# Optimization experiments

Hardware: AMD Instinct MI355X
Metric: run time of the kernel (lower is better)

The kernel has to match this reference:

```python
import jax, jax.numpy as jnp
import numpy as np

HIDDEN = 1024
EXPAND = 2
D_REC = HIDDEN * EXPAND
INTER = 4096
B, T = 4, 4096


def _rmsnorm(x, w, eps=1e-6):
    var = jnp.mean(x * x, axis=-1, keepdims=True)
    return x * jax.lax.rsqrt(var + eps) * w


def setup_inputs() -> dict:
    key = jax.random.key(0)
    ks = jax.random.split(key, 11)
    s = lambda fan: 1.0 / np.sqrt(fan)
    return {
        "x": jax.random.normal(ks[0], (B, T, HIDDEN), dtype=jnp.float32),
        "ln1_w": jnp.ones((HIDDEN,), dtype=jnp.float32),
        "ln2_w": jnp.ones((HIDDEN,), dtype=jnp.float32),
        "w_in": jax.random.normal(ks[1], (D_REC, HIDDEN), dtype=jnp.float32) * s(HIDDEN),
        "w_gate": jax.random.normal(ks[2], (D_REC, HIDDEN), dtype=jnp.float32) * s(HIDDEN),
        "a_param": jax.random.normal(ks[3], (D_REC,), dtype=jnp.float32) * 0.1,
        "w_a": jax.random.normal(ks[4], (D_REC, D_REC), dtype=jnp.float32) * s(D_REC),
        "w_out": jax.random.normal(ks[5], (HIDDEN, D_REC), dtype=jnp.float32) * s(D_REC),
        "w_mlp_gate": jax.random.normal(ks[6], (INTER, HIDDEN), dtype=jnp.float32) * s(HIDDEN),
        "w_mlp_up": jax.random.normal(ks[7], (INTER, HIDDEN), dtype=jnp.float32) * s(HIDDEN),
        "w_mlp_down": jax.random.normal(ks[8], (HIDDEN, INTER), dtype=jnp.float32) * s(INTER),
    }


def _hawk_scan(x_in, a):
    # x_in, a: [B, T, D_REC]; h_t = a_t*h_{t-1} + sqrt(1-a_t^2+eps)*x_t
    xs = jnp.moveaxis(x_in, 1, 0)  # [T, B, D]
    As = jnp.moveaxis(a, 1, 0)

    def step(state, inp):
        a_t, x_t = inp
        new = a_t * state + jnp.sqrt(1.0 - a_t * a_t + 1e-8) * x_t
        return new, new

    init = jnp.zeros(x_in.shape[::2], dtype=x_in.dtype)  # [B, D]
    _, ys = jax.lax.scan(step, init, (As, xs))
    return jnp.moveaxis(ys, 0, 1)  # [B, T, D]


def reference(x, ln1_w, ln2_w, w_in, w_gate, a_param, w_a, w_out,
              w_mlp_gate, w_mlp_up, w_mlp_down):
    h = _rmsnorm(x, ln1_w)
    x_in = h @ w_in.T                     # [B,T,D_REC]
    gate = jax.nn.sigmoid(h @ w_gate.T)
    a = jax.nn.sigmoid(a_param + x_in @ w_a.T)
    y = gate * _hawk_scan(x_in, a)
    x = x + y @ w_out.T
    h2 = _rmsnorm(x, ln2_w)
    mlp = (jax.nn.silu(h2 @ w_mlp_gate.T) * (h2 @ w_mlp_up.T)) @ w_mlp_down.T
    return x + mlp
```

## Files before the change

### kernel.cpp

```cpp
#include <hip/hip_runtime.h>
#include <cstdint>
#include <cmath>


typedef unsigned short u16;
typedef _Float16 f16;
typedef __bf16 bf16x8 __attribute__((ext_vector_type(8)));
typedef float  f32x4  __attribute__((ext_vector_type(4)));

#define HID   1024
#define DREC  2048
#define INTER 4096
#define BT    16384
#define TLEN  4096
#define NCHAN 8192
#define CHUNK 64
#define NCH   64
#define NPAIR 4096

__device__ __forceinline__ float b2f(u16 u) {
  union { unsigned int i; float f; } v; v.i = ((unsigned int)u) << 16; return v.f;
}
__device__ __forceinline__ u16 f2bf(float f) {
  unsigned int u = __builtin_bit_cast(unsigned int, f);
  u += 0x7FFFu + ((u >> 16) & 1u);
  return (u16)(u >> 16);
}
__device__ __forceinline__ float sigm(float x) { return 1.f / (1.f + expf(-x)); }

typedef __attribute__((address_space(1))) void as1_void;
typedef __attribute__((address_space(3))) void as3_void;
__device__ __forceinline__ void async16(const void* g, void* l) {
  __builtin_amdgcn_global_load_lds((as1_void*)g, (as3_void*)l, 16, 0, 0);
}

#define BARSYNC() do { __builtin_amdgcn_s_barrier(); __builtin_amdgcn_sched_barrier(0); } while (0)
#define LGKM0()   do { asm volatile("s_waitcnt lgkmcnt(0)" ::: "memory"); __builtin_amdgcn_sched_barrier(0); } while (0)
#define VMC(N)    do { asm volatile("s_waitcnt vmcnt(" #N ")" ::: "memory"); __builtin_amdgcn_sched_barrier(0); } while (0)
#define FENCE()   do { asm volatile("" ::: "memory"); __builtin_amdgcn_sched_barrier(0); } while (0)

__global__ void f2b_all(const float* s0, const float* s1, const float* s2,
                        const float* s3, const float* s4, const float* s5,
                        const float* s6,
                        u16* d0, u16* d1, u16* d2, u16* d3, u16* d4, u16* d5,
                        u16* d6) {
  int blk = blockIdx.x;
  const float* src; u16* dst; int rel;
  if      (blk < 2048)  { src = s0; dst = d0; rel = blk; }
  else if (blk < 4096)  { src = s1; dst = d1; rel = blk - 2048; }
  else if (blk < 8192)  { src = s2; dst = d2; rel = blk - 4096; }
  else if (blk < 10240) { src = s3; dst = d3; rel = blk - 8192; }
  else if (blk < 14336) { src = s4; dst = d4; rel = blk - 10240; }
  else if (blk < 18432) { src = s5; dst = d5; rel = blk - 14336; }
  else                  { src = s6; dst = d6; rel = blk - 18432; }
  int i = rel * 256 + threadIdx.x;
  float4 v = ((const float4*)src)[i];
  ushort4 o;
  o.x = f2bf(v.x); o.y = f2bf(v.y); o.z = f2bf(v.z); o.w = f2bf(v.w);
  ((ushort4*)dst)[i] = o;
}

__global__ void rmsnorm_kernel(const float* __restrict__ x, const float* __restrict__ w,
                               u16* __restrict__ out) {
  const int row = blockIdx.x;
  const int tid = threadIdx.x;
  float4 v = ((const float4*)(x + (size_t)row * HID))[tid];
  float ss = v.x * v.x + v.y * v.y + v.z * v.z + v.w * v.w;
#pragma unroll
  for (int o = 32; o > 0; o >>= 1) ss += __shfl_down(ss, o);
  __shared__ float red[4];
  const int lane = tid & 63, wv = tid >> 6;
  if (lane == 0) red[wv] = ss;
  __syncthreads();
  float tot = red[0] + red[1] + red[2] + red[3];
  float sc = rsqrtf(tot * (1.f / (float)HID) + 1e-6f);
  float4 wv4 = ((const float4*)w)[tid];
  ushort4 o;
  o.x = f2bf(v.x * sc * wv4.x); o.y = f2bf(v.y * sc * wv4.y);
  o.z = f2bf(v.z * sc * wv4.z); o.w = f2bf(v.w * sc * wv4.w);
  ((ushort4*)(out + (size_t)row * HID))[tid] = o;
}

__device__ __forceinline__ void stageG(const u16* __restrict__ g, int ldg,
                                       int rb, int k0, u16* lbase, int tid) {
#pragma unroll
  for (int i = 0; i < 2; ++i) {
    int p = i * 512 + tid;
    int r = p >> 3;
    int sg = (p & 7) ^ (r & 7);
    async16(g + (size_t)(rb + r) * ldg + (k0 + sg * 8), (char*)lbase + p * 16);
  }
}

__device__ __forceinline__ void readA4(bf16x8 (&af)[4][2], const u16* base,
                                       int rbase, int quad) {
#pragma unroll
  for (int i = 0; i < 4; ++i) {
    int r = rbase + i * 16;
#pragma unroll
    for (int ks = 0; ks < 2; ++ks)
      af[i][ks] = ((const bf16x8*)base)[r * 8 + ((ks * 4 + quad) ^ (r & 7))];
  }
}
__device__ __forceinline__ void readB2(bf16x8 (&bf)[2][2], const u16* base,
                                       int rbase, int quad) {
#pragma unroll
  for (int i = 0; i < 2; ++i) {
    int r = rbase + i * 16;
#pragma unroll
    for (int ks = 0; ks < 2; ++ks)
      bf[i][ks] = ((const bf16x8*)base)[r * 8 + ((ks * 4 + quad) ^ (r & 7))];
  }
}

template <int MI0, int NI0, int NA>
__device__ __forceinline__ void mfmaQ(f32x4 (&acc)[8][NA],
                                      const bf16x8 (&af)[4][2],
                                      const bf16x8 (&bf)[2][2]) {
  __builtin_amdgcn_s_setprio(1);
#pragma unroll
  for (int mi = 0; mi < 4; ++mi)
#pragma unroll
    for (int ni = 0; ni < 2; ++ni)
#pragma unroll
      for (int ks = 0; ks < 2; ++ks)
        acc[MI0 + mi][NI0 + ni] = __builtin_amdgcn_mfma_f32_16x16x32_bf16(
            af[mi][ks], bf[ni][ks], acc[MI0 + mi][NI0 + ni], 0, 0, 0);
  __builtin_amdgcn_s_setprio(0);
}

enum { EPI_LOGIT = 0, EPI_ADDF = 1 };

template <int EPI>
__global__ __launch_bounds__(512, 2)
void gemm256(const u16* __restrict__ A, const u16* __restrict__ W,
             int K, int N, int ldA, int ldW,
             float* outf, f16* outz, const float* auxf) {
  __shared__ u16 sA[2][16384];
  __shared__ u16 sB[2][16384];
  const int tid  = threadIdx.x;
  const int lane = tid & 63, wv = tid >> 6;
  const int wm   = wv >> 2, wn = wv & 3;
  const int lm   = lane & 15, quad = lane >> 4;
  const int row0 = blockIdx.x * 256, col0 = blockIdx.y * 256;
  const int NT   = K >> 6;

  f32x4 acc[8][4];
#pragma unroll
  for (int i = 0; i < 8; ++i)
#pragma unroll
    for (int j = 0; j < 4; ++j) acc[i][j] = (f32x4)0.f;

  stageG(W, ldW, col0,       0, sB[0],        tid);
  stageG(W, ldW, col0 + 128, 0, sB[0] + 8192, tid);
  stageG(A, ldA, row0,       0, sA[0],        tid);
  stageG(A, ldA, row0 + 128, 0, sA[0] + 8192, tid);
  FENCE();
  if (NT > 1) {
    stageG(W, ldW, col0,       64, sB[1],        tid);
    stageG(W, ldW, col0 + 128, 64, sB[1] + 8192, tid);
    stageG(A, ldA, row0,       64, sA[1],        tid);
    stageG(A, ldA, row0 + 128, 64, sA[1] + 8192, tid);
    VMC(8);
  } else {
    VMC(0);
  }
  BARSYNC();

  for (int t = 0; t < NT; ++t) {
    const int b = t & 1;
    const u16* Ab = sA[b];
    const u16* Bb = sB[b];
    bf16x8 af[4][2], bfL[2][2], bfH[2][2];
    const int kN = (t + 2) * 64;

    readA4(af, Ab, wm * 128 + lm, quad);
    readB2(bfL, Bb, wn * 64 + lm, quad);
    BARSYNC(); LGKM0();
    mfmaQ<0, 0>(acc, af, bfL);
    BARSYNC();

    readB2(bfH, Bb, wn * 64 + 32 + lm, quad);
    BARSYNC(); LGKM0();
    mfmaQ<0, 2>(acc, af, bfH);
    BARSYNC();

    readA4(af, Ab, wm * 128 + 64 + lm, quad);
    if (t + 2 < NT) {
      stageG(W, ldW, col0,       kN, (u16*)sB[b],        tid);
      stageG(W, ldW, col0 + 128, kN, (u16*)sB[b] + 8192, tid);
    }
    BARSYNC(); LGKM0();
    mfmaQ<4, 2>(acc, af, bfH);
    BARSYNC();

    if (t + 2 < NT) {
      stageG(A, ldA, row0,       kN, (u16*)sA[b],        tid);
      stageG(A, ldA, row0 + 128, kN, (u16*)sA[b] + 8192, tid);
    }
    mfmaQ<4, 0>(acc, af, bfL);
    if (t + 2 < NT) { VMC(8); } else { VMC(0); }
    BARSYNC();
  }

#pragma unroll
  for (int mi = 0; mi < 8; ++mi) {
    const int rb = row0 + wm * 128 + mi * 16 + quad * 4;
#pragma unroll
    for (int ni = 0; ni < 4; ++ni) {
      const int cg = col0 + wn * 64 + ni * 16 + lm;
      f32x4 v = acc[mi][ni];
#pragma unroll
      for (int rr = 0; rr < 4; ++rr) {
        size_t idx = (size_t)(rb + rr) * N + cg;
        if constexpr (EPI == EPI_LOGIT) {
          outz[idx] = (f16)(v[rr] + auxf[cg]);
        } else {
          outf[idx] = v[rr] + auxf[idx];
        }
      }
    }
  }
}

enum { EPI2_XG = 0, EPI2_SM = 1 };

template <int EPI>
__global__ __launch_bounds__(512, 2)
void gemm256d(const u16* __restrict__ A, const u16* __restrict__ W0,
              const u16* __restrict__ W1,
              int K, int N, int ldA, int ldW,
              u16* out0, u16* out1) {
  __shared__ u16 sA[2][16384];
  __shared__ u16 sB[2][16384];
  const int tid  = threadIdx.x;
  const int lane = tid & 63, wv = tid >> 6;
  const int wm   = wv >> 2, wn = wv & 3;
  const int lm   = lane & 15, quad = lane >> 4;
  const int row0 = blockIdx.x * 256, col0 = blockIdx.y * 128;
  const int NT   = K >> 6;

  f32x4 acc0[8][2], acc1[8][2];
#pragma unroll
  for (int i = 0; i < 8; ++i)
#pragma unroll
    for (int j = 0; j < 2; ++j) { acc0[i][j] = (f32x4)0.f; acc1[i][j] = (f32x4)0.f; }

  stageG(W0, ldW, col0,       0, sB[0],        tid);
  stageG(W1, ldW, col0,       0, sB[0] + 8192, tid);
  stageG(A,  ldA, row0,       0, sA[0],        tid);
  stageG(A,  ldA, row0 + 128, 0, sA[0] + 8192, tid);
  FENCE();
  if (NT > 1) {
    stageG(W0, ldW, col0,       64, sB[1],        tid);
    stageG(W1, ldW, col0,       64, sB[1] + 8192, tid);
    stageG(A,  ldA, row0,       64, sA[1],        tid);
    stageG(A,  ldA, row0 + 128, 64, sA[1] + 8192, tid);
    VMC(8);
  } else {
    VMC(0);
  }
  BARSYNC();

  for (int t = 0; t < NT; ++t) {
    const int b = t & 1;
    const u16* Ab = sA[b];
    const u16* Bb = sB[b];
    bf16x8 af[4][2], bf0[2][2], bf1[2][2];
    const int kN = (t + 2) * 64;

    readA4(af, Ab, wm * 128 + lm, quad);
    readB2(bf0, Bb, wn * 32 + lm, quad);
    BARSYNC(); LGKM0();
    mfmaQ<0, 0>(acc0, af, bf0);
    BARSYNC();

    readB2(bf1, Bb + 8192, wn * 32 + lm, quad);
    if (t + 2 < NT) stageG(W0, ldW, col0, kN, (u16*)sB[b], tid);
    BARSYNC(); LGKM0();
    mfmaQ<0, 0>(acc1, af, bf1);
    BARSYNC();

    readA4(af, Ab, wm * 128 + 64 + lm, quad);
    if (t + 2 < NT) stageG(W1, ldW, col0, kN, (u16*)sB[b] + 8192, tid);
    BARSYNC(); LGKM0();
    mfmaQ<4, 0>(acc1, af, bf1);
    BARSYNC();

    if (t + 2 < NT) {
      stageG(A, ldA, row0,       kN, (u16*)sA[b],        tid);
      stageG(A, ldA, row0 + 128, kN, (u16*)sA[b] + 8192, tid);
    }
    mfmaQ<4, 0>(acc0, af, bf0);
    if (t + 2 < NT) { VMC(8); } else { VMC(0); }
    BARSYNC();
  }

#pragma unroll
  for (int mi = 0; mi < 8; ++mi) {
    const int rb = row0 + wm * 128 + mi * 16 + quad * 4;
#pragma unroll
    for (int ni = 0; ni < 2; ++ni) {
      const int cg = col0 + wn * 32 + ni * 16 + lm;
#pragma unroll
      for (int rr = 0; rr < 4; ++rr) {
        size_t idx = (size_t)(rb + rr) * N + cg;
        float v0 = acc0[mi][ni][rr];
        float v1 = acc1[mi][ni][rr];
        if constexpr (EPI == EPI2_XG) {
          out0[idx] = f2bf(v0);
          out1[idx] = f2bf(sigm(v1));
        } else {
          out0[idx] = f2bf(v0 * sigm(v0) * v1);
        }
      }
    }
  }
}

__global__ void scan_phase1(const f16* __restrict__ z, const u16* __restrict__ xin,
                            float2* __restrict__ ch_h, float2* __restrict__ ch_p) {
  int gtid = blockIdx.x * 256 + threadIdx.x;
  int c = gtid >> 12;
  int pair = gtid & (NPAIR - 1);
  int b = pair >> 10;
  int d = (pair & 1023) * 2;
  size_t base = ((size_t)b * TLEN + (size_t)c * CHUNK) * DREC + d;
  float2 h = {0.f, 0.f}, P = {1.f, 1.f};
#pragma unroll 8
  for (int t = 0; t < CHUNK; ++t) {
    size_t i = base + (size_t)t * DREC;
    f16 z2[2]; *(uint32_t*)z2 = *(const uint32_t*)(z + i);
    u16 x2[2]; *(uint32_t*)x2 = *(const uint32_t*)(xin + i);
    float a0 = sigm((float)z2[0]), a1 = sigm((float)z2[1]);
    h.x = a0 * h.x + sqrtf(1.f - a0 * a0 + 1e-8f) * b2f(x2[0]);
    h.y = a1 * h.y + sqrtf(1.f - a1 * a1 + 1e-8f) * b2f(x2[1]);
    P.x *= a0; P.y *= a1;
  }
  ch_h[gtid] = h;
  ch_p[gtid] = P;
}

__global__ void scan_phase2(float2* __restrict__ ch_h, const float2* __restrict__ ch_p) {
  int pair = blockIdx.x * 256 + threadIdx.x;
  float2 H = {0.f, 0.f};
#pragma unroll
  for (int c = 0; c < NCH; ++c) {
    int i = c * NPAIR + pair;
    float2 he = ch_h[i];
    float2 P  = ch_p[i];
    ch_h[i] = H;
    H.x = he.x + P.x * H.x;
    H.y = he.y + P.y * H.y;
  }
}

__global__ void scan_phase3(const f16* __restrict__ z, const u16* __restrict__ xin,
                            u16* gate_y, const float2* __restrict__ ch_h) {
  int gtid = blockIdx.x * 256 + threadIdx.x;
  int c = gtid >> 12;
  int pair = gtid & (NPAIR - 1);
  int b = pair >> 10;
  int d = (pair & 1023) * 2;
  size_t base = ((size_t)b * TLEN + (size_t)c * CHUNK) * DREC + d;
  float2 h = ch_h[gtid];
#pragma unroll 8
  for (int t = 0; t < CHUNK; ++t) {
    size_t i = base + (size_t)t * DREC;
    f16 z2[2]; *(uint32_t*)z2 = *(const uint32_t*)(z + i);
    u16 x2[2]; *(uint32_t*)x2 = *(const uint32_t*)(xin + i);
    u16 g2[2]; *(uint32_t*)g2 = *(const uint32_t*)(gate_y + i);
    float a0 = sigm((float)z2[0]), a1 = sigm((float)z2[1]);
    h.x = a0 * h.x + sqrtf(1.f - a0 * a0 + 1e-8f) * b2f(x2[0]);
    h.y = a1 * h.y + sqrtf(1.f - a1 * a1 + 1e-8f) * b2f(x2[1]);
    u16 o2[2];
    o2[0] = f2bf(b2f(g2[0]) * h.x);
    o2[1] = f2bf(b2f(g2[1]) * h.y);
    *(uint32_t*)(gate_y + i) = *(uint32_t*)o2;
  }
}

extern "C" void kernel_launch(void* const* d_in, const int* in_sizes, int n_in,
                              void* d_out, int out_size, void* d_ws, size_t ws_size,
                              hipStream_t stream) {
  const float* x      = (const float*)d_in[0];
  const float* ln1    = (const float*)d_in[1];
  const float* ln2    = (const float*)d_in[2];
  const float* w_in   = (const float*)d_in[3];
  const float* w_gate = (const float*)d_in[4];
  const float* a_par  = (const float*)d_in[5];
  const float* w_a    = (const float*)d_in[6];
  const float* w_out  = (const float*)d_in[7];
  const float* w_mg   = (const float*)d_in[8];
  const float* w_mu   = (const float*)d_in[9];
  const float* w_md   = (const float*)d_in[10];
  float* out = (float*)d_out;
  char* ws = (char*)d_ws;

  const size_t MB = 1024ull * 1024ull;
  u16* wb_in  = (u16*)(ws + 0 * MB);
  u16* wb_gt  = (u16*)(ws + 4 * MB);
  u16* wb_a   = (u16*)(ws + 8 * MB);
  u16* wb_out = (u16*)(ws + 16 * MB);
  u16* wb_mg  = (u16*)(ws + 20 * MB);
  u16* wb_mu  = (u16*)(ws + 28 * MB);
  u16* wb_md  = (u16*)(ws + 36 * MB);
  u16* hbuf  = (u16*)(ws + 44 * MB);
  f16* zbuf  = (f16*)(ws + 44 * MB);
  u16* gateb = (u16*)(ws + 108 * MB);
  u16* mbuf  = (u16*)(ws + 108 * MB);
  float2* chh = (float2*)(ws + 0 * MB);
  float2* chp = (float2*)(ws + 2 * MB);
  u16* xinb = (u16*)d_out;

  f2b_all<<<22528, 256, 0, stream>>>(w_in, w_gate, w_a, w_out, w_mg, w_mu, w_md,
                                     wb_in, wb_gt, wb_a, wb_out, wb_mg, wb_mu, wb_md);

  rmsnorm_kernel<<<BT, 256, 0, stream>>>(x, ln1, hbuf);

  gemm256d<EPI2_XG><<<dim3(BT / 256, DREC / 128), 512, 0, stream>>>(
      hbuf, wb_in, wb_gt, HID, DREC, HID, HID, xinb, gateb);

  gemm256<EPI_LOGIT><<<dim3(BT / 256, DREC / 256), 512, 0, stream>>>(
      xinb, wb_a, DREC, DREC, DREC, DREC, nullptr, zbuf, a_par);

  scan_phase1<<<NCH * NPAIR / 256, 256, 0, stream>>>(zbuf, xinb, chh, chp);
  scan_phase2<<<NPAIR / 256, 256, 0, stream>>>(chh, chp);
  scan_phase3<<<NCH * NPAIR / 256, 256, 0, stream>>>(zbuf, xinb, gateb, chh);

  gemm256<EPI_ADDF><<<dim3(BT / 256, HID / 256), 512, 0, stream>>>(
      gateb, wb_out, DREC, HID, DREC, DREC, out, nullptr, x);

  rmsnorm_kernel<<<BT, 256, 0, stream>>>(out, ln2, hbuf);

  for (int half = 0; half < 2; ++half) {
    const u16* wmg_h = wb_mg + (size_t)half * 2048 * HID;
    const u16* wmu_h = wb_mu + (size_t)half * 2048 * HID;
    const u16* wmd_h = wb_md + (size_t)half * 2048;
    gemm256d<EPI2_SM><<<dim3(BT / 256, 2048 / 64 / 2), 512, 0, stream>>>(
        hbuf, wmg_h, wmu_h, HID, 2048, HID, HID, mbuf, nullptr);
    gemm256<EPI_ADDF><<<dim3(BT / 256, HID / 256), 512, 0, stream>>>(
        mbuf, wmd_h, 2048, HID, 2048, INTER, out, nullptr, out);
  }
}
```

Before: 1.210 ms.

## Batch LDS fragment reads and cut barriers in GEMM main loops

In both the single-output and dual-output GEMM main loops, all A and B fragments for a k-step are now read from LDS up front into separate low and high register sets. The explicit lgkmcnt waits are dropped and the compiler inserts the waits itself. The per-iteration barrier count falls from seven to three, so LDS reads and MFMAs can overlap more freely. The cost is extra VGPRs for the duplicated A fragments, which could lower occupancy or cause spills. The MLP launch grid expression is rewritten but evaluates to the same value.

Result: no change. 1.192 ms (-1.5%).

```diff
diff --git a/kernel.cpp b/kernel.cpp
--- a/kernel.cpp
+++ b/kernel.cpp
@@ -35,7 +35,6 @@
 }
 
 #define BARSYNC() do { __builtin_amdgcn_s_barrier(); __builtin_amdgcn_sched_barrier(0); } while (0)
-#define LGKM0()   do { asm volatile("s_waitcnt lgkmcnt(0)" ::: "memory"); __builtin_amdgcn_sched_barrier(0); } while (0)
 #define VMC(N)    do { asm volatile("s_waitcnt vmcnt(" #N ")" ::: "memory"); __builtin_amdgcn_sched_barrier(0); } while (0)
 #define FENCE()   do { asm volatile("" ::: "memory"); __builtin_amdgcn_sched_barrier(0); } while (0)
 
@@ -171,34 +170,30 @@
     const int b = t & 1;
     const u16* Ab = sA[b];
     const u16* Bb = sB[b];
-    bf16x8 af[4][2], bfL[2][2], bfH[2][2];
+    bf16x8 afL[4][2], afH[4][2], bfL[2][2], bfH[2][2];
     const int kN = (t + 2) * 64;
 
-    readA4(af, Ab, wm * 128 + lm, quad);
+    readA4(afL, Ab, wm * 128 + lm, quad);
     readB2(bfL, Bb, wn * 64 + lm, quad);
-    BARSYNC(); LGKM0();
-    mfmaQ<0, 0>(acc, af, bfL);
-    BARSYNC();
-
     readB2(bfH, Bb, wn * 64 + 32 + lm, quad);
-    BARSYNC(); LGKM0();
-    mfmaQ<0, 2>(acc, af, bfH);
-    BARSYNC();
-
-    readA4(af, Ab, wm * 128 + 64 + lm, quad);
+    readA4(afH, Ab, wm * 128 + 64 + lm, quad);
+
+    mfmaQ<0, 0>(acc, afL, bfL);
+    mfmaQ<0, 2>(acc, afL, bfH);
+
+    BARSYNC();
     if (t + 2 < NT) {
       stageG(W, ldW, col0,       kN, (u16*)sB[b],        tid);
       stageG(W, ldW, col0 + 128, kN, (u16*)sB[b] + 8192, tid);
     }
-    BARSYNC(); LGKM0();
-    mfmaQ<4, 2>(acc, af, bfH);
-    BARSYNC();
-
+    mfmaQ<4, 2>(acc, afH, bfH);
+
+    BARSYNC();
     if (t + 2 < NT) {
       stageG(A, ldA, row0,       kN, (u16*)sA[b],        tid);
       stageG(A, ldA, row0 + 128, kN, (u16*)sA[b] + 8192, tid);
     }
-    mfmaQ<4, 0>(acc, af, bfL);
+    mfmaQ<4, 0>(acc, afH, bfL);
     if (t + 2 < NT) { VMC(8); } else { VMC(0); }
     BARSYNC();
   }
@@ -266,32 +261,30 @@
     const int b = t & 1;
     const u16* Ab = sA[b];
     const u16* Bb = sB[b];
-    bf16x8 af[4][2], bf0[2][2], bf1[2][2];
+    bf16x8 afL[4][2], afH[4][2], bf0[2][2], bf1[2][2];
     const int kN = (t + 2) * 64;
 
-    readA4(af, Ab, wm * 128 + lm, quad);
+    readA4(afL, Ab, wm * 128 + lm, quad);
     readB2(bf0, Bb, wn * 32 + lm, quad);
-    BARSYNC(); LGKM0();
-    mfmaQ<0, 0>(acc0, af, bf0);
-    BARSYNC();
-
     readB2(bf1, Bb + 8192, wn * 32 + lm, quad);
-    if (t + 2 < NT) stageG(W0, ldW, col0, kN, (u16*)sB[b], tid);
-    BARSYNC(); LGKM0();
-    mfmaQ<0, 0>(acc1, af, bf1);
-    BARSYNC();
-
-    readA4(af, Ab, wm * 128 + 64 + lm, quad);
-    if (t + 2 < NT) stageG(W1, ldW, col0, kN, (u16*)sB[b] + 8192, tid);
-    BARSYNC(); LGKM0();
-    mfmaQ<4, 0>(acc1, af, bf1);
-    BARSYNC();
-
+    readA4(afH, Ab, wm * 128 + 64 + lm, quad);
+
+    mfmaQ<0, 0>(acc0, afL, bf0);
+    mfmaQ<0, 0>(acc1, afL, bf1);
+
+    BARSYNC();
+    if (t + 2 < NT) {
+      stageG(W0, ldW, col0, kN, (u16*)sB[b],        tid);
+      stageG(W1, ldW, col0, kN, (u16*)sB[b] + 8192, tid);
+    }
+    mfmaQ<4, 0>(acc1, afH, bf1);
+
+    BARSYNC();
     if (t + 2 < NT) {
       stageG(A, ldA, row0,       kN, (u16*)sA[b],        tid);
       stageG(A, ldA, row0 + 128, kN, (u16*)sA[b] + 8192, tid);
     }
-    mfmaQ<4, 0>(acc0, af, bf0);
+    mfmaQ<4, 0>(acc0, afH, bf0);
     if (t + 2 < NT) { VMC(8); } else { VMC(0); }
     BARSYNC();
   }
@@ -437,7 +430,7 @@
     const u16* wmg_h = wb_mg + (size_t)half * 2048 * HID;
     const u16* wmu_h = wb_mu + (size_t)half * 2048 * HID;
     const u16* wmd_h = wb_md + (size_t)half * 2048;
-    gemm256d<EPI2_SM><<<dim3(BT / 256, 2048 / 64 / 2), 512, 0, stream>>>(
+    gemm256d<EPI2_SM><<<dim3(BT / 256, 2048 / 128), 512, 0, stream>>>(
         hbuf, wmg_h, wmu_h, HID, 2048, HID, HID, mbuf, nullptr);
     gemm256<EPI_ADDF><<<dim3(BT / 256, HID / 256), 512, 0, stream>>>(
         mbuf, wmd_h, 2048, HID, 2048, INTER, out, nullptr, out);
```
